# Kernel tuning notes

Measured on AMD Instinct MI355X. Metric: run time of the kernel, lower is better.

Reference implementation:

```python
import jax, jax.numpy as jnp
import numpy as np

NHEAD = 8

def layernorm(x, g, b, eps=1e-5):
    mu = x.mean(-1, keepdims=True)
    var = ((x - mu) ** 2).mean(-1, keepdims=True)
    return (x - mu) / jnp.sqrt(var + eps) * g + b

def linear_attention(q, k, v, eps=1e-6):
    # LoFTR kernelized linear attention: phi(x) = elu(x) + 1
    Q = jax.nn.elu(q) + 1.0          # [n, l, h, d]
    K = jax.nn.elu(k) + 1.0          # [n, s, h, d]
    s_len = v.shape[1]
    KV = jnp.einsum("nshd,nshv->nhdv", K, v / s_len)
    Z = 1.0 / (jnp.einsum("nlhd,nhd->nlh", Q, K.sum(axis=1)) + eps)
    return jnp.einsum("nlhd,nhdv,nlh->nlhv", Q, KV, Z) * s_len

def _block(x_base, q, k, v, Wm, W1, W2, g1, b1, g2, b2):
    bs, L, h, dh = q.shape
    msg = linear_attention(q, k, v).reshape(bs, L, h * dh)
    msg = layernorm(msg @ Wm, g1, b1)
    hcat = jnp.concatenate([x_base, msg], axis=2)          # [bs, L, 2*d]
    out = jax.nn.relu(hcat @ W1) @ W2
    return layernorm(out, g2, b2)

def setup_inputs() -> dict:
    key = jax.random.key(0)
    ks = jax.random.split(key, 8)
    bs, L, S, d = 8, 4800, 4800, 256
    w = lambda k, i, o: jax.random.normal(k, (i, o), jnp.float32) * 0.02
    return {
        "x": jax.random.normal(ks[0], (bs, L, d), jnp.float32),
        "source": jax.random.normal(ks[1], (bs, S, d), jnp.float32),
        "Wq": w(ks[2], d, d), "Wk": w(ks[3], d, d), "Wv": w(ks[4], d, d),
        "Wm": w(ks[5], d, d),
        "W1": w(ks[6], 2 * d, 2 * d), "W2": w(ks[7], 2 * d, d),
        "g1": jnp.ones((d,), jnp.float32), "b1": jnp.zeros((d,), jnp.float32),
        "g2": jnp.ones((d,), jnp.float32), "b2": jnp.zeros((d,), jnp.float32),
    }

def reference(x, source, Wq, Wk, Wv, Wm, W1, W2, g1, b1, g2, b2):
    bs, L, d = x.shape
    h = NHEAD
    dh = d // h
    q = (x @ Wq).reshape(bs, L, h, dh)
    k = (source @ Wk).reshape(bs, -1, h, dh)
    v = (source @ Wv).reshape(bs, -1, h, dh)
    # permute-then-view reinterpretations, exactly as in the torch code
    p13 = lambda t: t.transpose(0, 1, 3, 2).reshape(bs, -1, h, dh)  # permute(0,1,3,2)
    p21 = lambda t: t.transpose(0, 2, 1, 3).reshape(bs, -1, h, dh)  # permute(0,2,1,3)
    p32 = lambda t: t.transpose(0, 3, 2, 1).reshape(bs, -1, h, dh)  # permute(0,3,2,1)
    blk = lambda xb, qq, kk, vv: _block(xb, qq, kk, vv, Wm, W1, W2, g1, b1, g2, b2)
    m = blk(x, q, k, v)
    m3 = blk(x, p13(q), p13(k), p13(v))
    x_mid = x + 0.5 * (m + m3)
    m1 = blk(x_mid, p21(q), p21(k), p21(v))
    m2 = blk(x_mid, p32(q), p32(k), p32(v))
    return x_mid + 0.5 * (m1 + m2)
```

## Files before the change

kernel.cpp:

```cpp
#include <hip/hip_runtime.h>
#include <type_traits>
#include <cstdint>
#include <cstddef>

#define L_SEQ 4800
#define DMODEL 256
#define BS 8
#define MROWS (BS*L_SEQ)
#define PERBATCH (L_SEQ*DMODEL)
#define KVSET 67584

typedef __attribute__((ext_vector_type(8))) short bfrag8;
typedef __attribute__((ext_vector_type(4))) float floatx4;

__device__ __forceinline__ float bf2f(unsigned short u){
  union { unsigned int i; float f; } x; x.i = ((unsigned int)u) << 16; return x.f;
}
__device__ __forceinline__ unsigned short f2bf(float f){
  union { float f; unsigned int i; } x; x.f = f;
  x.i += 0x7fff + ((x.i >> 16) & 1);
  return (unsigned short)(x.i >> 16);
}
__device__ __forceinline__ float phi(float x){
  return x > 0.f ? x + 1.f : __expf(x);
}
__device__ __forceinline__ void gll16(const void* g, void* l){
  __builtin_amdgcn_global_load_lds((const __attribute__((address_space(1))) unsigned int*)g,
      (__attribute__((address_space(3))) unsigned int*)l, 16, 0, 0);
}

template<typename TC, bool RELU>
__global__ __launch_bounds__(256) void gemm_mfma(const unsigned short* __restrict__ A,
                                                 const unsigned short* __restrict__ Bt,
                                                 TC* __restrict__ C, int M, int N, int K){
  __shared__ unsigned short Al[128*32];
  __shared__ unsigned short Bl[128*32];
  const int tid  = threadIdx.x;
  const int lane = tid & 63;
  const int wave = tid >> 6;
  const int row0 = blockIdx.y << 7;
  const int col0 = blockIdx.x << 7;
  const int wr0  = (wave & 1) << 6;
  const int wc0  = (wave >> 1) << 6;

  floatx4 acc[4][4] = {};

  const int i0 = tid, i1 = tid + 256;
  const int r0 = i0 >> 2, s0 = i0 & 3;
  const int r1 = i1 >> 2, s1 = i1 & 3;
  const int m = lane & 15, q = lane >> 4;

  for (int k0 = 0; k0 < K; k0 += 32){
    const unsigned short* ga0 = A  + (size_t)(row0 + r0)*K + k0 + s0*8;
    const unsigned short* ga1 = A  + (size_t)(row0 + r1)*K + k0 + s1*8;
    const unsigned short* gb0 = Bt + (size_t)(col0 + r0)*K + k0 + s0*8;
    const unsigned short* gb1 = Bt + (size_t)(col0 + r1)*K + k0 + s1*8;
    gll16(ga0, Al + (size_t)i0*8);
    gll16(ga1, Al + (size_t)i1*8);
    gll16(gb0, Bl + (size_t)i0*8);
    gll16(gb1, Bl + (size_t)i1*8);
    __builtin_amdgcn_s_waitcnt(0);
    __syncthreads();

    bfrag8 af[4], bf[4];
    #pragma unroll
    for (int t = 0; t < 4; t++){
      af[t] = *(const bfrag8*)(Al + (size_t)(wr0 + t*16 + m)*32 + q*8);
      bf[t] = *(const bfrag8*)(Bl + (size_t)(wc0 + t*16 + m)*32 + q*8);
    }
    #pragma unroll
    for (int mt = 0; mt < 4; mt++)
      #pragma unroll
      for (int nt = 0; nt < 4; nt++)
        acc[mt][nt] = __builtin_amdgcn_mfma_f32_16x16x32_bf16(af[mt], bf[nt], acc[mt][nt], 0, 0, 0);
    __syncthreads();
  }

  #pragma unroll
  for (int mt = 0; mt < 4; mt++){
    #pragma unroll
    for (int nt = 0; nt < 4; nt++){
      const int col  = col0 + wc0 + nt*16 + m;
      const int rowb = row0 + wr0 + mt*16 + q*4;
      #pragma unroll
      for (int i = 0; i < 4; i++){
        float v = acc[mt][nt][i];
        if (RELU) v = v > 0.f ? v : 0.f;
        if constexpr (std::is_same<TC,float>::value) C[(size_t)(rowb+i)*N + col] = v;
        else                                         C[(size_t)(rowb+i)*N + col] = f2bf(v);
      }
    }
  }
}

__global__ __launch_bounds__(256) void wconv(const float* __restrict__ W, unsigned short* __restrict__ Wt,
                                             int kshift, int N){
  int idx = blockIdx.x*256 + threadIdx.x;
  int kk = idx & ((1 << kshift) - 1);
  int nn = idx >> kshift;
  Wt[idx] = f2bf(W[(size_t)kk*N + nn]);
}
__global__ __launch_bounds__(256) void conv_bf16(const float* __restrict__ in, unsigned short* __restrict__ out){
  int i = blockIdx.x*256 + threadIdx.x;
  float4 v = ((const float4*)in)[i];
  ushort4 o; o.x = f2bf(v.x); o.y = f2bf(v.y); o.z = f2bf(v.z); o.w = f2bf(v.w);
  ((ushort4*)out)[i] = o;
}

__global__ __launch_bounds__(256) void permute1(const unsigned short* __restrict__ sA, unsigned short* __restrict__ dA,
                                                const unsigned short* __restrict__ sB, unsigned short* __restrict__ dB){
  const unsigned short* s = blockIdx.z ? sB : sA;
  unsigned short*       d = blockIdx.z ? dB : dA;
  __shared__ unsigned short tile[1024];
  const int t = threadIdx.x;
  const size_t base = (size_t)blockIdx.x * 1024;
  #pragma unroll
  for (int i = 0; i < 4; i++) tile[i*256 + t] = s[base + i*256 + t];
  __syncthreads();
  const int pg = ((t & 7) << 5) + (t >> 3);
  #pragma unroll
  for (int i = 0; i < 4; i++) d[base + i*256 + t] = tile[i*256 + pg];
}

__global__ __launch_bounds__(256) void permute2(const unsigned short* __restrict__ sA, unsigned short* __restrict__ dA,
                                                const unsigned short* __restrict__ sB, unsigned short* __restrict__ dB){
  const unsigned short* s = blockIdx.z ? sB : sA;
  unsigned short*       d = blockIdx.z ? dB : dA;
  __shared__ unsigned short tile[64*256];
  const int t = threadIdx.x;
  const int rr0 = blockIdx.x * 64;
  const size_t boff = (size_t)blockIdx.y * PERBATCH;
  #pragma unroll
  for (int i = 0; i < 16; i++){
    int u = i*256 + t;
    *(ushort4*)&tile[u*4] = *(const ushort4*)&s[boff + (size_t)rr0*256 + (size_t)u*4];
  }
  __syncthreads();
  #pragma unroll
  for (int i = 0; i < 8; i++){
    #pragma unroll
    for (int w = 0; w < 2; w++){
      int u = w*256 + t;
      int rr = u >> 3, c4 = (u & 7) << 2;
      ushort4 v = *(const ushort4*)&tile[rr*256 + i*32 + c4];
      *(ushort4*)&d[boff + (size_t)i*153600 + (size_t)rr0*32 + (size_t)u*4] = v;
    }
  }
}

__global__ __launch_bounds__(256) void permute3(const unsigned short* __restrict__ sA, unsigned short* __restrict__ dA,
                                                const unsigned short* __restrict__ sB, unsigned short* __restrict__ dB){
  const unsigned short* s = blockIdx.z ? sB : sA;
  unsigned short*       d = blockIdx.z ? dB : dA;
  __shared__ unsigned short tile[64*258];
  const int t = threadIdx.x;
  const int ll0 = blockIdx.x * 64;
  const size_t boff = (size_t)blockIdx.y * PERBATCH;
  #pragma unroll
  for (int i = 0; i < 32; i++){
    int u = i*256 + t;
    int row = u >> 7, col = (u & 127) << 1;
    *(ushort2*)&tile[row*258 + col] = *(const ushort2*)&s[boff + (size_t)(ll0+row)*256 + col];
  }
  __syncthreads();
  const int cw = t >> 6;
  const int ll = t & 63;
  #pragma unroll
  for (int cc = 0; cc < 256; cc += 4){
    int c = cc + cw;
    int sigma = ((c & 31) << 3) + (c >> 5);
    d[boff + (size_t)sigma*4800 + ll0 + ll] = tile[ll*258 + c];
  }
}

__global__ __launch_bounds__(256) void attn_stats(const unsigned short* __restrict__ kq,
                                                  const unsigned short* __restrict__ vq,
                                                  float* __restrict__ KV, float* __restrict__ Ksum){
  const int chunk = blockIdx.x, h = blockIdx.y, n = blockIdx.z;
  const int t = threadIdx.x;
  const int d = t >> 3;
  const int w4 = (t & 7) << 2;
  const size_t boff = (size_t)n * PERBATCH;
  __shared__ float kb[8][32], vb[8][32];
  const int lr = t >> 5, lj = t & 31;
  float a0=0.f, a1=0.f, a2=0.f, a3=0.f, ks=0.f;
  const int s0 = chunk * 240;
  for (int s = s0; s < s0 + 240; s += 8){
    int srci = (s + lr)*256 + (h << 5) + lj;
    kb[lr][lj] = phi(bf2f(kq[boff + srci]));
    vb[lr][lj] = bf2f(vq[boff + srci]);
    __syncthreads();
    #pragma unroll
    for (int r = 0; r < 8; r++){
      float kd = kb[r][d];
      ks += kd;
      a0 += kd * vb[r][w4+0];
      a1 += kd * vb[r][w4+1];
      a2 += kd * vb[r][w4+2];
      a3 += kd * vb[r][w4+3];
    }
    __syncthreads();
  }
  float* kvp = KV + (size_t)((((n<<3)+h)<<5) + d)*32 + w4;
  atomicAdd(kvp+0, a0);
  atomicAdd(kvp+1, a1);
  atomicAdd(kvp+2, a2);
  atomicAdd(kvp+3, a3);
  if ((t & 7) == 0) atomicAdd(Ksum + (((n<<3)+h)<<5) + d, ks);
}

__global__ __launch_bounds__(256) void attn_fused(const unsigned short* __restrict__ qq,
                                                  const float* __restrict__ KV,
                                                  const float* __restrict__ Ksum,
                                                  const unsigned short* __restrict__ WmT,
                                                  const float* __restrict__ g1,
                                                  const float* __restrict__ b1,
                                                  unsigned short* __restrict__ hcat){
  __shared__ float kvs[8192];
  __shared__ char  msgL[32768];
  __shared__ char  pool[16384];
  const int t = threadIdx.x;
  const int n = blockIdx.y;
  const int row0 = blockIdx.x << 6;
  const size_t boff = (size_t)n * PERBATCH;

  #pragma unroll
  for (int i = 0; i < 32; i++) kvs[i*256 + t] = KV[(size_t)n*8192 + i*256 + t];
  const float kssv = Ksum[n*256 + t];

  const int h = t >> 5, w = t & 31;
  const float* kvh = kvs + h*1024;
  float* Qs = (float*)pool;

  for (int p = 0; p < 8; p++){
    #pragma unroll
    for (int r = 0; r < 8; r++)
      Qs[r*256 + t] = phi(bf2f(qq[boff + (size_t)(row0 + p*8 + r)*256 + t]));
    __syncthreads();

    float acc[8], den[8];
    #pragma unroll
    for (int r = 0; r < 8; r++){
      float dd = Qs[r*256 + t] * kssv;
      #pragma unroll
      for (int o = 1; o < 32; o <<= 1) dd += __shfl_xor(dd, o, 64);
      den[r] = dd + 1e-6f;
      acc[r] = 0.f;
    }
    #pragma unroll
    for (int d4 = 0; d4 < 8; d4++){
      const float k0v = kvh[(d4*4+0)*32 + w];
      const float k1v = kvh[(d4*4+1)*32 + w];
      const float k2v = kvh[(d4*4+2)*32 + w];
      const float k3v = kvh[(d4*4+3)*32 + w];
      #pragma unroll
      for (int r = 0; r < 8; r++){
        float4 qv = *(const float4*)&Qs[r*256 + h*32 + d4*4];
        acc[r] += qv.x*k0v + qv.y*k1v + qv.z*k2v + qv.w*k3v;
      }
    }
    #pragma unroll
    for (int r = 0; r < 8; r++){
      int lrow = p*8 + r;
      int byte = (lrow << 9) + (t << 1);
      byte ^= (lrow & 7) << 4;
      *(unsigned short*)(msgL + byte) = f2bf(acc[r] / den[r]);
    }
    __syncthreads();
  }

  const int wave = t >> 6, lane = t & 63, m = lane & 15, qd = lane >> 4;
  float gv[16], bv[16];
  #pragma unroll
  for (int nt = 0; nt < 16; nt++){ gv[nt] = g1[nt*16 + m]; bv[nt] = b1[nt*16 + m]; }

  floatx4 acc[16] = {};
  for (int ks = 0; ks < 8; ks++){
    const int k0 = ks << 5;
    #pragma unroll
    for (int i = 0; i < 4; i++){
      int u = (i << 8) + t;
      int c = u >> 2, q4 = u & 3;
      gll16(WmT + (size_t)c*256 + k0 + ((q4 ^ (c & 3)) << 3), pool + (u << 4));
    }
    asm volatile("s_waitcnt vmcnt(0)" ::: "memory");
    __builtin_amdgcn_s_barrier();
    asm volatile("" ::: "memory");
    const int arow = (wave << 4) + m;
    int abyte = (arow << 9) + (ks << 6) + (qd << 4);
    abyte ^= (m & 7) << 4;
    bfrag8 af = *(const bfrag8*)(msgL + abyte);
    #pragma unroll
    for (int nt = 0; nt < 16; nt++){
      int col = (nt << 4) + m;
      bfrag8 bf = *(const bfrag8*)(pool + col*64 + ((qd ^ (m & 3)) << 4));
      acc[nt] = __builtin_amdgcn_mfma_f32_16x16x32_bf16(af, bf, acc[nt], 0, 0, 0);
    }
    asm volatile("" ::: "memory");
    __builtin_amdgcn_s_barrier();
    asm volatile("" ::: "memory");
  }

  float mu[4], rs[4];
  #pragma unroll
  for (int i = 0; i < 4; i++){
    float s = 0.f, q = 0.f;
    #pragma unroll
    for (int nt = 0; nt < 16; nt++){ float v = acc[nt][i]; s += v; q += v*v; }
    #pragma unroll
    for (int o = 1; o < 16; o <<= 1){ s += __shfl_xor(s, o, 64); q += __shfl_xor(q, o, 64); }
    float mean = s * (1.f/256.f);
    float var  = q * (1.f/256.f) - mean*mean;
    mu[i] = mean; rs[i] = rsqrtf(var + 1e-5f);
  }
  #pragma unroll
  for (int nt = 0; nt < 16; nt++){
    #pragma unroll
    for (int i = 0; i < 4; i++){
      int row = (wave << 4) + (qd << 2) + i;
      int col = (nt << 4) + m;
      int byte = (row << 9) + (col << 1);
      byte ^= (row & 7) << 4;
      *(unsigned short*)(msgL + byte) = f2bf((acc[nt][i] - mu[i]) * rs[i] * gv[nt] + bv[nt]);
    }
  }
  __syncthreads();
  const size_t gbase = (size_t)(n*4800 + row0) * 512;
  #pragma unroll
  for (int i = 0; i < 16; i++){
    int u = (i << 8) + t;
    int row = u >> 6, j = u & 63;
    int byte = ((row << 9) + (j << 3)) ^ ((row & 7) << 4);
    *(ushort4*)(hcat + gbase + (size_t)row*512 + 256 + (j << 2)) = *(const ushort4*)(msgL + byte);
  }
}

__global__ __launch_bounds__(512) void ffn_fused(const unsigned short* __restrict__ hcat,
                                                 const unsigned short* __restrict__ W1T,
                                                 const unsigned short* __restrict__ W2T,
                                                 const float* __restrict__ g2,
                                                 const float* __restrict__ b2,
                                                 float* __restrict__ macc, int add){
  __shared__ char stg[73728];
  __shared__ char hidm[65536];
  const int tid = threadIdx.x;
  const int wave = tid >> 6, lane = tid & 63;
  const int rg = wave >> 1, ch = wave & 1;
  const int m = lane & 15, qd = lane >> 4;
  const int row0 = blockIdx.x << 6;

  float gv[8], bv[8];
  #pragma unroll
  for (int nt = 0; nt < 8; nt++){
    int col = (ch << 7) + nt*16 + m;
    gv[nt] = g2[col]; bv[nt] = b2[col];
  }

  auto stage1 = [&](int ks, int b){
    const int k0 = ks << 5;
    {
      int u = tid & 255;
      int r = u >> 2, q4 = u & 3;
      gll16(hcat + (size_t)(row0 + r)*512 + k0 + ((q4 ^ (r & 3)) << 3),
            stg + (b << 12) + (u << 4));
    }
    #pragma unroll
    for (int i = 0; i < 4; i++){
      int u = (i << 9) + tid;
      int c = u >> 2, q4 = u & 3;
      gll16(W1T + (size_t)c*512 + k0 + ((q4 ^ (c & 3)) << 3),
            stg + 8192 + (b << 15) + (u << 4));
    }
  };

  floatx4 acc1[16] = {};
  stage1(0, 0);
  asm volatile("s_waitcnt vmcnt(0)" ::: "memory");
  __builtin_amdgcn_s_barrier();
  asm volatile("" ::: "memory");
  for (int ks = 0; ks < 16; ks++){
    if (ks < 15) stage1(ks+1, (ks+1) & 1);
    const char* hb = stg + ((ks & 1) << 12);
    const char* wb = stg + 8192 + ((ks & 1) << 15);
    const int arow = (rg << 4) + m;
    bfrag8 af = *(const bfrag8*)(hb + arow*64 + ((qd ^ (m & 3)) << 4));
    #pragma unroll
    for (int nt = 0; nt < 16; nt++){
      int col = (ch << 8) + (nt << 4) + m;
      bfrag8 bf = *(const bfrag8*)(wb + col*64 + ((qd ^ (m & 3)) << 4));
      acc1[nt] = __builtin_amdgcn_mfma_f32_16x16x32_bf16(af, bf, acc1[nt], 0, 0, 0);
    }
    asm volatile("" ::: "memory");
    if (ks < 15) asm volatile("s_waitcnt vmcnt(0)" ::: "memory");
    __builtin_amdgcn_s_barrier();
    asm volatile("" ::: "memory");
  }

  #pragma unroll
  for (int nt = 0; nt < 16; nt++){
    #pragma unroll
    for (int i = 0; i < 4; i++){
      float v = acc1[nt][i];
      v = v > 0.f ? v : 0.f;
      int row = (rg << 4) + (qd << 2) + i;
      int col = (ch << 8) + (nt << 4) + m;
      int byte = (row << 10) + (col << 1);
      byte ^= (row & 7) << 4;
      *(unsigned short*)(hidm + byte) = f2bf(v);
    }
  }

  auto stage2 = [&](int ks, int b){
    const int k0 = ks << 5;
    #pragma unroll
    for (int i = 0; i < 2; i++){
      int u = (i << 9) + tid;
      int c = u >> 2, q4 = u & 3;
      gll16(W2T + (size_t)c*512 + k0 + ((q4 ^ (c & 3)) << 3),
            stg + (b << 14) + (u << 4));
    }
  };
  stage2(0, 0);
  asm volatile("s_waitcnt vmcnt(0) lgkmcnt(0)" ::: "memory");
  __builtin_amdgcn_s_barrier();
  asm volatile("" ::: "memory");

  floatx4 acc2[8] = {};
  for (int ks = 0; ks < 16; ks++){
    if (ks < 15) stage2(ks+1, (ks+1) & 1);
    const char* wb = stg + ((ks & 1) << 14);
    const int arow = (rg << 4) + m;
    int abyte = (arow << 10) + (ks << 6) + (qd << 4);
    abyte ^= (m & 7) << 4;
    bfrag8 af = *(const bfrag8*)(hidm + abyte);
    #pragma unroll
    for (int nt = 0; nt < 8; nt++){
      int col = (ch << 7) + (nt << 4) + m;
      bfrag8 bf = *(const bfrag8*)(wb + col*64 + ((qd ^ (m & 3)) << 4));
      acc2[nt] = __builtin_amdgcn_mfma_f32_16x16x32_bf16(af, bf, acc2[nt], 0, 0, 0);
    }
    asm volatile("" ::: "memory");
    if (ks < 15) asm volatile("s_waitcnt vmcnt(0)" ::: "memory");
    __builtin_amdgcn_s_barrier();
    asm volatile("" ::: "memory");
  }

  float2* LNp = (float2*)(stg + 32768);
  #pragma unroll
  for (int i = 0; i < 4; i++){
    float s = 0.f, q = 0.f;
    #pragma unroll
    for (int nt = 0; nt < 8; nt++){ float v = acc2[nt][i]; s += v; q += v*v; }
    #pragma unroll
    for (int o = 1; o < 16; o <<= 1){ s += __shfl_xor(s, o, 64); q += __shfl_xor(q, o, 64); }
    if (m == 0){
      int row = (rg << 4) + (qd << 2) + i;
      LNp[row*2 + ch] = make_float2(s, q);
    }
  }
  asm volatile("s_waitcnt lgkmcnt(0)" ::: "memory");
  __builtin_amdgcn_s_barrier();
  asm volatile("" ::: "memory");

  float mu[4], rs[4];
  #pragma unroll
  for (int i = 0; i < 4; i++){
    int row = (rg << 4) + (qd << 2) + i;
    float2 a = LNp[row*2], c = LNp[row*2 + 1];
    float S = a.x + c.x, Q = a.y + c.y;
    float mean = S * (1.f/256.f);
    float var  = Q * (1.f/256.f) - mean*mean;
    mu[i] = mean; rs[i] = rsqrtf(var + 1e-5f);
  }
  float* ysh = (float*)hidm;
  #pragma unroll
  for (int nt = 0; nt < 8; nt++){
    #pragma unroll
    for (int i = 0; i < 4; i++){
      int row = (rg << 4) + (qd << 2) + i;
      int col = (ch << 7) + (nt << 4) + m;
      ysh[(row << 8) + col] = (acc2[nt][i] - mu[i]) * rs[i] * gv[nt] + bv[nt];
    }
  }
  asm volatile("s_waitcnt lgkmcnt(0)" ::: "memory");
  __builtin_amdgcn_s_barrier();
  asm volatile("" ::: "memory");
  #pragma unroll
  for (int i = 0; i < 8; i++){
    int u = (i << 9) + tid;
    int row = u >> 6, c4 = u & 63;
    float4 v = *(const float4*)(ysh + (row << 8) + (c4 << 2));
    float4* gp = (float4*)(macc + (size_t)(row0 + row)*256) + c4;
    if (add){ float4 o = *gp; v.x += o.x; v.y += o.y; v.z += o.z; v.w += o.w; }
    *gp = v;
  }
}

__global__ __launch_bounds__(256) void fill_hcat(const float* __restrict__ x, unsigned short* __restrict__ hcat){
  size_t i = (size_t)blockIdx.x*256 + threadIdx.x;
  hcat[(i >> 8)*512 + (i & 255)] = f2bf(x[i]);
}
__global__ __launch_bounds__(256) void xmid_k(const float* __restrict__ x, const float* __restrict__ macc,
                                              float* __restrict__ xmid, unsigned short* __restrict__ hcat){
  size_t i = (size_t)blockIdx.x*256 + threadIdx.x;
  float v = x[i] + 0.5f*macc[i];
  xmid[i] = v;
  hcat[(i >> 8)*512 + (i & 255)] = f2bf(v);
}
__global__ __launch_bounds__(256) void final_k(float* __restrict__ out, const float* __restrict__ macc){
  size_t i = (size_t)blockIdx.x*256 + threadIdx.x;
  out[i] = out[i] + 0.5f*macc[i];
}
__global__ __launch_bounds__(256) void zero_k(float* __restrict__ p, int n){
  int i = blockIdx.x*256 + threadIdx.x;
  if (i < n) p[i] = 0.f;
}

extern "C" void kernel_launch(void* const* d_in, const int* in_sizes, int n_in,
                              void* d_out, int out_size, void* d_ws, size_t ws_size,
                              hipStream_t stream){
  const float* x   = (const float*)d_in[0];
  const float* src = (const float*)d_in[1];
  const float* Wq  = (const float*)d_in[2];
  const float* Wk  = (const float*)d_in[3];
  const float* Wv  = (const float*)d_in[4];
  const float* Wm  = (const float*)d_in[5];
  const float* W1  = (const float*)d_in[6];
  const float* W2  = (const float*)d_in[7];
  const float* g1  = (const float*)d_in[8];
  const float* b1  = (const float*)d_in[9];
  const float* g2  = (const float*)d_in[10];
  const float* b2  = (const float*)d_in[11];
  float* out = (float*)d_out;

  char* ws = (char*)d_ws;
  size_t off = 0;
  auto alloc = [&](size_t bytes) -> void* {
    void* p = ws + off;
    off += (bytes + 255) & ~(size_t)255;
    return p;
  };
  unsigned short* qB    = (unsigned short*)alloc((size_t)MROWS*256*2);
  unsigned short* kB    = (unsigned short*)alloc((size_t)MROWS*256*2);
  unsigned short* vB    = (unsigned short*)alloc((size_t)MROWS*256*2);
  unsigned short* hcatB = (unsigned short*)alloc((size_t)MROWS*512*2);
  float* t1   = (float*)alloc((size_t)MROWS*256*4);
  float* macc = (float*)alloc((size_t)MROWS*256*4);
  float* KV4  = (float*)alloc((size_t)4*KVSET*4);
  unsigned short* WqT = (unsigned short*)alloc((size_t)256*256*2);
  unsigned short* WkT = (unsigned short*)alloc((size_t)256*256*2);
  unsigned short* WvT = (unsigned short*)alloc((size_t)256*256*2);
  unsigned short* WmT = (unsigned short*)alloc((size_t)256*256*2);
  unsigned short* W1T = (unsigned short*)alloc((size_t)512*512*2);
  unsigned short* W2T = (unsigned short*)alloc((size_t)256*512*2);
  (void)ws_size; (void)in_sizes; (void)n_in; (void)out_size;

  unsigned short* srcbf = (unsigned short*)t1;
  unsigned short* xbf   = srcbf + (size_t)MROWS*256;
  unsigned short* qP    = (unsigned short*)t1;
  unsigned short* kP    = (unsigned short*)macc;
  unsigned short* vP    = kP + (size_t)MROWS*256;
  float* xmid = out;

  const dim3 blk(256);

  wconv<<<dim3(256),  blk, 0, stream>>>(Wq, WqT, 8, 256);
  wconv<<<dim3(256),  blk, 0, stream>>>(Wk, WkT, 8, 256);
  wconv<<<dim3(256),  blk, 0, stream>>>(Wv, WvT, 8, 256);
  wconv<<<dim3(256),  blk, 0, stream>>>(Wm, WmT, 8, 256);
  wconv<<<dim3(1024), blk, 0, stream>>>(W1, W1T, 9, 512);
  wconv<<<dim3(512),  blk, 0, stream>>>(W2, W2T, 9, 256);
  conv_bf16<<<dim3(9600), blk, 0, stream>>>(src, srcbf);
  conv_bf16<<<dim3(9600), blk, 0, stream>>>(x,   xbf);

  gemm_mfma<unsigned short, false><<<dim3(2,300), blk, 0, stream>>>(xbf,   WqT, qB, MROWS, 256, 256);
  gemm_mfma<unsigned short, false><<<dim3(2,300), blk, 0, stream>>>(srcbf, WkT, kB, MROWS, 256, 256);
  gemm_mfma<unsigned short, false><<<dim3(2,300), blk, 0, stream>>>(srcbf, WvT, vB, MROWS, 256, 256);

  zero_k<<<dim3(1056), blk, 0, stream>>>(KV4, 4*KVSET);
  attn_stats<<<dim3(20,8,8), blk, 0, stream>>>(kB, vB, KV4 + 0*KVSET, KV4 + 0*KVSET + 65536);
  permute1<<<dim3(9600,1,2), blk, 0, stream>>>(kB, kP, vB, vP);
  attn_stats<<<dim3(20,8,8), blk, 0, stream>>>(kP, vP, KV4 + 1*KVSET, KV4 + 1*KVSET + 65536);
  permute2<<<dim3(75,8,2),  blk, 0, stream>>>(kB, kP, vB, vP);
  attn_stats<<<dim3(20,8,8), blk, 0, stream>>>(kP, vP, KV4 + 2*KVSET, KV4 + 2*KVSET + 65536);
  permute3<<<dim3(75,8,2),  blk, 0, stream>>>(kB, kP, vB, vP);
  attn_stats<<<dim3(20,8,8), blk, 0, stream>>>(kP, vP, KV4 + 3*KVSET, KV4 + 3*KVSET + 65536);

  fill_hcat<<<dim3(MROWS), blk, 0, stream>>>(x, hcatB);

  auto run_block = [&](int mode, int add){
    const float* KV   = KV4 + (size_t)mode*KVSET;
    const float* Ksum = KV + 65536;
    const unsigned short* qsrc = qB;
    if (mode == 1){ permute1<<<dim3(9600,1,1), blk, 0, stream>>>(qB, qP, nullptr, nullptr); qsrc = qP; }
    else if (mode == 2){ permute2<<<dim3(75,8,1), blk, 0, stream>>>(qB, qP, nullptr, nullptr); qsrc = qP; }
    else if (mode == 3){ permute3<<<dim3(75,8,1), blk, 0, stream>>>(qB, qP, nullptr, nullptr); qsrc = qP; }
    attn_fused<<<dim3(75,BS), blk, 0, stream>>>(qsrc, KV, Ksum, WmT, g1, b1, hcatB);
    ffn_fused<<<dim3(600), dim3(512), 0, stream>>>(hcatB, W1T, W2T, g2, b2, macc, add);
  };

  run_block(0, 0);
  run_block(1, 1);
  xmid_k<<<dim3(MROWS), blk, 0, stream>>>(x, macc, xmid, hcatB);
  run_block(2, 0);
  run_block(3, 1);
  final_k<<<dim3(MROWS), blk, 0, stream>>>(out, macc);
}
```

Baseline: 1.108 ms.

## Double-buffer GEMM, shrink attention tiles, restructure fused FFN to cut LDS use

The generic GEMM now double-buffers its LDS tiles with XOR swizzling and uses one barrier per k-step. The attention kernel drops from 64 to 16 rows per block with 4x more blocks. It computes the denominator inline from a shared Ksum and reads Wm fragments straight from global memory. The FFN kernel drops its 64KB hidden buffer and streams hidden-activation chunks through the staging buffer while W2 loads, with each wave owning a column slice and launch bounds asking for more occupancy. Together these aim to raise occupancy and overlap, at the cost of more complex producer scheduling and redundant global Wm reads per block.

```diff
diff --git a/kernel.cpp b/kernel.cpp
--- a/kernel.cpp
+++ b/kernel.cpp
@@ -33,8 +33,8 @@
 __global__ __launch_bounds__(256) void gemm_mfma(const unsigned short* __restrict__ A,
                                                  const unsigned short* __restrict__ Bt,
                                                  TC* __restrict__ C, int M, int N, int K){
-  __shared__ unsigned short Al[128*32];
-  __shared__ unsigned short Bl[128*32];
+  __shared__ unsigned short Al[2][4096];
+  __shared__ unsigned short Bl[2][4096];
   const int tid  = threadIdx.x;
   const int lane = tid & 63;
   const int wave = tid >> 6;
@@ -42,38 +42,42 @@
   const int col0 = blockIdx.x << 7;
   const int wr0  = (wave & 1) << 6;
   const int wc0  = (wave >> 1) << 6;
+  const int m = lane & 15, q = lane >> 4;
+  const int sw = (m >> 1) & 3;
 
   floatx4 acc[4][4] = {};
 
-  const int i0 = tid, i1 = tid + 256;
-  const int r0 = i0 >> 2, s0 = i0 & 3;
-  const int r1 = i1 >> 2, s1 = i1 & 3;
-  const int m = lane & 15, q = lane >> 4;
-
-  for (int k0 = 0; k0 < K; k0 += 32){
-    const unsigned short* ga0 = A  + (size_t)(row0 + r0)*K + k0 + s0*8;
-    const unsigned short* ga1 = A  + (size_t)(row0 + r1)*K + k0 + s1*8;
-    const unsigned short* gb0 = Bt + (size_t)(col0 + r0)*K + k0 + s0*8;
-    const unsigned short* gb1 = Bt + (size_t)(col0 + r1)*K + k0 + s1*8;
-    gll16(ga0, Al + (size_t)i0*8);
-    gll16(ga1, Al + (size_t)i1*8);
-    gll16(gb0, Bl + (size_t)i0*8);
-    gll16(gb1, Bl + (size_t)i1*8);
-    __builtin_amdgcn_s_waitcnt(0);
-    __syncthreads();
-
+  const int u0 = tid, u1 = tid + 256;
+  const int r0 = u0 >> 2, s0 = u0 & 3;
+  const int r1 = u1 >> 2, s1 = u1 & 3;
+
+  auto stage = [&](int k0, int b){
+    gll16(A  + (size_t)(row0 + r0)*K + k0 + ((s0 ^ ((r0 >> 1) & 3)) << 3), Al[b] + (size_t)u0*8);
+    gll16(A  + (size_t)(row0 + r1)*K + k0 + ((s1 ^ ((r1 >> 1) & 3)) << 3), Al[b] + (size_t)u1*8);
+    gll16(Bt + (size_t)(col0 + r0)*K + k0 + ((s0 ^ ((r0 >> 1) & 3)) << 3), Bl[b] + (size_t)u0*8);
+    gll16(Bt + (size_t)(col0 + r1)*K + k0 + ((s1 ^ ((r1 >> 1) & 3)) << 3), Bl[b] + (size_t)u1*8);
+  };
+
+  stage(0, 0);
+  const int nk = K >> 5;
+  for (int ks = 0; ks < nk; ks++){
+    asm volatile("s_waitcnt vmcnt(0) lgkmcnt(0)" ::: "memory");
+    __builtin_amdgcn_s_barrier();
+    asm volatile("" ::: "memory");
+    if (ks < nk - 1) stage((ks + 1) << 5, (ks + 1) & 1);
+    const unsigned short* ab = Al[ks & 1];
+    const unsigned short* bb = Bl[ks & 1];
     bfrag8 af[4], bf[4];
     #pragma unroll
     for (int t = 0; t < 4; t++){
-      af[t] = *(const bfrag8*)(Al + (size_t)(wr0 + t*16 + m)*32 + q*8);
-      bf[t] = *(const bfrag8*)(Bl + (size_t)(wc0 + t*16 + m)*32 + q*8);
+      af[t] = *(const bfrag8*)(ab + (size_t)(wr0 + t*16 + m)*32 + ((q ^ sw) << 3));
+      bf[t] = *(const bfrag8*)(bb + (size_t)(wc0 + t*16 + m)*32 + ((q ^ sw) << 3));
     }
     #pragma unroll
     for (int mt = 0; mt < 4; mt++)
       #pragma unroll
       for (int nt = 0; nt < 4; nt++)
         acc[mt][nt] = __builtin_amdgcn_mfma_f32_16x16x32_bf16(af[mt], bf[nt], acc[mt][nt], 0, 0, 0);
-    __syncthreads();
   }
 
   #pragma unroll
@@ -217,283 +221,276 @@
                                                   const float* __restrict__ b1,
                                                   unsigned short* __restrict__ hcat){
   __shared__ float kvs[8192];
-  __shared__ char  msgL[32768];
-  __shared__ char  pool[16384];
+  __shared__ float Qs[4096];
+  __shared__ float kss[256];
+  __shared__ char  msgL[8192];
+  __shared__ float2 LNp[16][4];
   const int t = threadIdx.x;
   const int n = blockIdx.y;
-  const int row0 = blockIdx.x << 6;
+  const int row0 = blockIdx.x << 4;
   const size_t boff = (size_t)n * PERBATCH;
 
-  #pragma unroll
-  for (int i = 0; i < 32; i++) kvs[i*256 + t] = KV[(size_t)n*8192 + i*256 + t];
-  const float kssv = Ksum[n*256 + t];
-
-  const int h = t >> 5, w = t & 31;
-  const float* kvh = kvs + h*1024;
-  float* Qs = (float*)pool;
-
-  for (int p = 0; p < 8; p++){
-    #pragma unroll
-    for (int r = 0; r < 8; r++)
-      Qs[r*256 + t] = phi(bf2f(qq[boff + (size_t)(row0 + p*8 + r)*256 + t]));
-    __syncthreads();
-
-    float acc[8], den[8];
-    #pragma unroll
-    for (int r = 0; r < 8; r++){
-      float dd = Qs[r*256 + t] * kssv;
-      #pragma unroll
-      for (int o = 1; o < 32; o <<= 1) dd += __shfl_xor(dd, o, 64);
-      den[r] = dd + 1e-6f;
-      acc[r] = 0.f;
-    }
-    #pragma unroll
-    for (int d4 = 0; d4 < 8; d4++){
-      const float k0v = kvh[(d4*4+0)*32 + w];
-      const float k1v = kvh[(d4*4+1)*32 + w];
-      const float k2v = kvh[(d4*4+2)*32 + w];
-      const float k3v = kvh[(d4*4+3)*32 + w];
-      #pragma unroll
-      for (int r = 0; r < 8; r++){
-        float4 qv = *(const float4*)&Qs[r*256 + h*32 + d4*4];
-        acc[r] += qv.x*k0v + qv.y*k1v + qv.z*k2v + qv.w*k3v;
-      }
-    }
-    #pragma unroll
-    for (int r = 0; r < 8; r++){
-      int lrow = p*8 + r;
-      int byte = (lrow << 9) + (t << 1);
-      byte ^= (lrow & 7) << 4;
-      *(unsigned short*)(msgL + byte) = f2bf(acc[r] / den[r]);
-    }
-    __syncthreads();
-  }
-
-  const int wave = t >> 6, lane = t & 63, m = lane & 15, qd = lane >> 4;
-  float gv[16], bv[16];
-  #pragma unroll
-  for (int nt = 0; nt < 16; nt++){ gv[nt] = g1[nt*16 + m]; bv[nt] = b1[nt*16 + m]; }
-
-  floatx4 acc[16] = {};
-  for (int ks = 0; ks < 8; ks++){
-    const int k0 = ks << 5;
+  {
+    const float4* kvsrc = (const float4*)(KV + (size_t)n*8192);
+    #pragma unroll
+    for (int i = 0; i < 8; i++) ((float4*)kvs)[i*256 + t] = kvsrc[i*256 + t];
+    kss[t] = Ksum[n*256 + t];
     #pragma unroll
     for (int i = 0; i < 4; i++){
       int u = (i << 8) + t;
-      int c = u >> 2, q4 = u & 3;
-      gll16(WmT + (size_t)c*256 + k0 + ((q4 ^ (c & 3)) << 3), pool + (u << 4));
-    }
-    asm volatile("s_waitcnt vmcnt(0)" ::: "memory");
-    __builtin_amdgcn_s_barrier();
-    asm volatile("" ::: "memory");
-    const int arow = (wave << 4) + m;
-    int abyte = (arow << 9) + (ks << 6) + (qd << 4);
-    abyte ^= (m & 7) << 4;
+      int r = u >> 6, c4 = (u & 63) << 2;
+      ushort4 v = *(const ushort4*)(qq + boff + (size_t)(row0 + r)*256 + c4);
+      float4 f;
+      f.x = phi(bf2f(v.x)); f.y = phi(bf2f(v.y)); f.z = phi(bf2f(v.z)); f.w = phi(bf2f(v.w));
+      *(float4*)&Qs[r*256 + c4] = f;
+    }
+  }
+  __syncthreads();
+
+  {
+    const int h = t >> 5, w = t & 31;
+    const float* kvh = kvs + h*1024;
+    const float* ksh = kss + h*32;
+    float acc[16], den[16];
+    #pragma unroll
+    for (int r = 0; r < 16; r++){ acc[r] = 0.f; den[r] = 1e-6f; }
+    #pragma unroll
+    for (int d4 = 0; d4 < 8; d4++){
+      const float k0 = kvh[(d4*4+0)*32 + w];
+      const float k1 = kvh[(d4*4+1)*32 + w];
+      const float k2 = kvh[(d4*4+2)*32 + w];
+      const float k3 = kvh[(d4*4+3)*32 + w];
+      const float s0 = ksh[d4*4+0], s1 = ksh[d4*4+1], s2 = ksh[d4*4+2], s3 = ksh[d4*4+3];
+      #pragma unroll
+      for (int r = 0; r < 16; r++){
+        float4 qv = *(const float4*)&Qs[r*256 + h*32 + d4*4];
+        acc[r] += qv.x*k0 + qv.y*k1 + qv.z*k2 + qv.w*k3;
+        den[r] += qv.x*s0 + qv.y*s1 + qv.z*s2 + qv.w*s3;
+      }
+    }
+    #pragma unroll
+    for (int r = 0; r < 16; r++){
+      int byte = (r << 9) + ((t << 1) ^ ((r & 7) << 4));
+      *(unsigned short*)(msgL + byte) = f2bf(acc[r] / den[r]);
+    }
+  }
+  __syncthreads();
+
+  const int wv = t >> 6, lane = t & 63, m = lane & 15, qd = lane >> 4;
+  floatx4 Cf[4] = {};
+  #pragma unroll
+  for (int ks = 0; ks < 8; ks++){
+    int abyte = m*512 + ((ks*64 + qd*16) ^ ((m & 7) << 4));
     bfrag8 af = *(const bfrag8*)(msgL + abyte);
     #pragma unroll
-    for (int nt = 0; nt < 16; nt++){
-      int col = (nt << 4) + m;
-      bfrag8 bf = *(const bfrag8*)(pool + col*64 + ((qd ^ (m & 3)) << 4));
-      acc[nt] = __builtin_amdgcn_mfma_f32_16x16x32_bf16(af, bf, acc[nt], 0, 0, 0);
-    }
-    asm volatile("" ::: "memory");
-    __builtin_amdgcn_s_barrier();
-    asm volatile("" ::: "memory");
-  }
-
-  float mu[4], rs[4];
+    for (int nt = 0; nt < 4; nt++){
+      int col = wv*64 + nt*16 + m;
+      bfrag8 bf = *(const bfrag8*)(WmT + (size_t)col*256 + ks*32 + qd*8);
+      Cf[nt] = __builtin_amdgcn_mfma_f32_16x16x32_bf16(af, bf, Cf[nt], 0, 0, 0);
+    }
+  }
+
   #pragma unroll
   for (int i = 0; i < 4; i++){
     float s = 0.f, q = 0.f;
     #pragma unroll
-    for (int nt = 0; nt < 16; nt++){ float v = acc[nt][i]; s += v; q += v*v; }
+    for (int nt = 0; nt < 4; nt++){ float v = Cf[nt][i]; s += v; q += v*v; }
     #pragma unroll
     for (int o = 1; o < 16; o <<= 1){ s += __shfl_xor(s, o, 64); q += __shfl_xor(q, o, 64); }
-    float mean = s * (1.f/256.f);
-    float var  = q * (1.f/256.f) - mean*mean;
-    mu[i] = mean; rs[i] = rsqrtf(var + 1e-5f);
-  }
-  #pragma unroll
-  for (int nt = 0; nt < 16; nt++){
-    #pragma unroll
-    for (int i = 0; i < 4; i++){
-      int row = (wave << 4) + (qd << 2) + i;
-      int col = (nt << 4) + m;
-      int byte = (row << 9) + (col << 1);
-      byte ^= (row & 7) << 4;
-      *(unsigned short*)(msgL + byte) = f2bf((acc[nt][i] - mu[i]) * rs[i] * gv[nt] + bv[nt]);
-    }
-  }
-  __syncthreads();
-  const size_t gbase = (size_t)(n*4800 + row0) * 512;
-  #pragma unroll
-  for (int i = 0; i < 16; i++){
+    if (m == 0) LNp[qd*4 + i][wv] = make_float2(s, q);
+  }
+  __syncthreads();
+  float gv[4], bv[4];
+  #pragma unroll
+  for (int nt = 0; nt < 4; nt++){ int col = wv*64 + nt*16 + m; gv[nt] = g1[col]; bv[nt] = b1[col]; }
+  #pragma unroll
+  for (int i = 0; i < 4; i++){
+    int row = qd*4 + i;
+    float2 p0 = LNp[row][0], p1 = LNp[row][1], p2 = LNp[row][2], p3 = LNp[row][3];
+    float S = p0.x + p1.x + p2.x + p3.x;
+    float Q = p0.y + p1.y + p2.y + p3.y;
+    float mu = S * (1.f/256.f);
+    float rs = rsqrtf(Q * (1.f/256.f) - mu*mu + 1e-5f);
+    #pragma unroll
+    for (int nt = 0; nt < 4; nt++){
+      int col = wv*64 + nt*16 + m;
+      *(unsigned short*)(msgL + row*512 + col*2) = f2bf((Cf[nt][i] - mu) * rs * gv[nt] + bv[nt]);
+    }
+  }
+  __syncthreads();
+  const size_t gbase = ((size_t)n*4800 + row0)*512 + 256;
+  #pragma unroll
+  for (int i = 0; i < 4; i++){
     int u = (i << 8) + t;
-    int row = u >> 6, j = u & 63;
-    int byte = ((row << 9) + (j << 3)) ^ ((row & 7) << 4);
-    *(ushort4*)(hcat + gbase + (size_t)row*512 + 256 + (j << 2)) = *(const ushort4*)(msgL + byte);
-  }
-}
-
-__global__ __launch_bounds__(512) void ffn_fused(const unsigned short* __restrict__ hcat,
-                                                 const unsigned short* __restrict__ W1T,
-                                                 const unsigned short* __restrict__ W2T,
-                                                 const float* __restrict__ g2,
-                                                 const float* __restrict__ b2,
-                                                 float* __restrict__ macc, int add){
+    int r = u >> 6, c4 = (u & 63) << 2;
+    *(ushort4*)(hcat + gbase + (size_t)r*512 + c4) = *(const ushort4*)(msgL + r*512 + c4*2);
+  }
+}
+
+__global__ __launch_bounds__(512, 4) void ffn_fused(const unsigned short* __restrict__ hcat,
+                                                    const unsigned short* __restrict__ W1T,
+                                                    const unsigned short* __restrict__ W2T,
+                                                    const float* __restrict__ g2,
+                                                    const float* __restrict__ b2,
+                                                    float* __restrict__ macc, int add){
   __shared__ char stg[73728];
-  __shared__ char hidm[65536];
   const int tid = threadIdx.x;
-  const int wave = tid >> 6, lane = tid & 63;
-  const int rg = wave >> 1, ch = wave & 1;
+  const int wv = tid >> 6, lane = tid & 63;
   const int m = lane & 15, qd = lane >> 4;
+  const int sw = (m >> 1) & 3;
   const int row0 = blockIdx.x << 6;
-
-  float gv[8], bv[8];
-  #pragma unroll
-  for (int nt = 0; nt < 8; nt++){
-    int col = (ch << 7) + nt*16 + m;
-    gv[nt] = g2[col]; bv[nt] = b2[col];
-  }
 
   auto stage1 = [&](int ks, int b){
     const int k0 = ks << 5;
     {
       int u = tid & 255;
       int r = u >> 2, q4 = u & 3;
-      gll16(hcat + (size_t)(row0 + r)*512 + k0 + ((q4 ^ (r & 3)) << 3),
+      gll16(hcat + (size_t)(row0 + r)*512 + k0 + ((q4 ^ ((r >> 1) & 3)) << 3),
             stg + (b << 12) + (u << 4));
     }
     #pragma unroll
     for (int i = 0; i < 4; i++){
       int u = (i << 9) + tid;
-      int c = u >> 2, q4 = u & 3;
-      gll16(W1T + (size_t)c*512 + k0 + ((q4 ^ (c & 3)) << 3),
+      int r = u >> 2, q4 = u & 3;
+      gll16(W1T + (size_t)r*512 + k0 + ((q4 ^ ((r >> 1) & 3)) << 3),
             stg + 8192 + (b << 15) + (u << 4));
     }
   };
 
-  floatx4 acc1[16] = {};
+  floatx4 acc1[4][4] = {};
   stage1(0, 0);
-  asm volatile("s_waitcnt vmcnt(0)" ::: "memory");
-  __builtin_amdgcn_s_barrier();
-  asm volatile("" ::: "memory");
   for (int ks = 0; ks < 16; ks++){
-    if (ks < 15) stage1(ks+1, (ks+1) & 1);
+    asm volatile("s_waitcnt vmcnt(0) lgkmcnt(0)" ::: "memory");
+    __builtin_amdgcn_s_barrier();
+    asm volatile("" ::: "memory");
+    if (ks < 15) stage1(ks + 1, (ks + 1) & 1);
     const char* hb = stg + ((ks & 1) << 12);
     const char* wb = stg + 8192 + ((ks & 1) << 15);
-    const int arow = (rg << 4) + m;
-    bfrag8 af = *(const bfrag8*)(hb + arow*64 + ((qd ^ (m & 3)) << 4));
-    #pragma unroll
-    for (int nt = 0; nt < 16; nt++){
-      int col = (ch << 8) + (nt << 4) + m;
-      bfrag8 bf = *(const bfrag8*)(wb + col*64 + ((qd ^ (m & 3)) << 4));
-      acc1[nt] = __builtin_amdgcn_mfma_f32_16x16x32_bf16(af, bf, acc1[nt], 0, 0, 0);
-    }
-    asm volatile("" ::: "memory");
-    if (ks < 15) asm volatile("s_waitcnt vmcnt(0)" ::: "memory");
+    bfrag8 af[4], bf[4];
+    #pragma unroll
+    for (int t = 0; t < 4; t++){
+      af[t] = *(const bfrag8*)(hb + (t*16 + m)*64 + ((qd ^ sw) << 4));
+      bf[t] = *(const bfrag8*)(wb + (wv*64 + t*16 + m)*64 + ((qd ^ sw) << 4));
+    }
+    #pragma unroll
+    for (int mt = 0; mt < 4; mt++)
+      #pragma unroll
+      for (int nt = 0; nt < 4; nt++)
+        acc1[mt][nt] = __builtin_amdgcn_mfma_f32_16x16x32_bf16(af[mt], bf[nt], acc1[mt][nt], 0, 0, 0);
+  }
+
+  unsigned int hp[4][4][2];
+  #pragma unroll
+  for (int mt = 0; mt < 4; mt++)
+    #pragma unroll
+    for (int nt = 0; nt < 4; nt++)
+      #pragma unroll
+      for (int i2 = 0; i2 < 2; i2++){
+        float a = acc1[mt][nt][2*i2];     a = a > 0.f ? a : 0.f;
+        float c = acc1[mt][nt][2*i2+1];   c = c > 0.f ? c : 0.f;
+        hp[mt][nt][i2] = (unsigned int)f2bf(a) | ((unsigned int)f2bf(c) << 16);
+      }
+
+#define PRODUCE_HALF(CB, NT0)                                                        \
+  { _Pragma("unroll")                                                                \
+    for (int mt = 0; mt < 4; mt++){                                                  \
+      _Pragma("unroll")                                                              \
+      for (int j = 0; j < 2; j++){                                                   \
+        _Pragma("unroll")                                                            \
+        for (int i = 0; i < 4; i++){                                                 \
+          int row = mt*16 + qd*4 + i;                                                \
+          int kl  = j*16 + m;                                                        \
+          int byte = row*64 + ((((kl >> 3)) ^ ((row >> 1) & 3)) << 4) + ((kl & 7) << 1); \
+          unsigned short v = (unsigned short)(hp[mt][(NT0) + j][i >> 1] >> ((i & 1) << 4)); \
+          *(unsigned short*)((CB) + byte) = v;                                       \
+        }                                                                            \
+      }                                                                              \
+    }                                                                                \
+  }
+
+  auto produce = [&](int c){
+    if (wv == (c >> 1)){
+      char* cb = stg + ((c & 1) << 12);
+      if ((c & 1) == 0) PRODUCE_HALF(cb, 0)
+      else              PRODUCE_HALF(cb, 2)
+    }
+  };
+  auto stage2 = [&](int ks, int b){
+    const int k0 = ks << 5;
+    #pragma unroll
+    for (int i = 0; i < 2; i++){
+      int u = (i << 9) + tid;
+      int r = u >> 2, q4 = u & 3;
+      gll16(W2T + (size_t)r*512 + k0 + ((q4 ^ ((r >> 1) & 3)) << 3),
+            stg + 8192 + (b << 14) + (u << 4));
+    }
+  };
+
+  produce(0);
+  stage2(0, 0);
+  floatx4 acc2[4][2] = {};
+  for (int ks = 0; ks < 16; ks++){
+    asm volatile("s_waitcnt vmcnt(0) lgkmcnt(0)" ::: "memory");
     __builtin_amdgcn_s_barrier();
     asm volatile("" ::: "memory");
-  }
-
-  #pragma unroll
-  for (int nt = 0; nt < 16; nt++){
+    if (ks < 15){ stage2(ks + 1, (ks + 1) & 1); produce(ks + 1); }
+    const char* cb = stg + ((ks & 1) << 12);
+    const char* wb = stg + 8192 + ((ks & 1) << 14);
+    bfrag8 af[4], bf[2];
+    #pragma unroll
+    for (int t = 0; t < 4; t++)
+      af[t] = *(const bfrag8*)(cb + (t*16 + m)*64 + ((qd ^ sw) << 4));
+    #pragma unroll
+    for (int nt = 0; nt < 2; nt++)
+      bf[nt] = *(const bfrag8*)(wb + (wv*32 + nt*16 + m)*64 + ((qd ^ sw) << 4));
+    #pragma unroll
+    for (int mt = 0; mt < 4; mt++)
+      #pragma unroll
+      for (int nt = 0; nt < 2; nt++)
+        acc2[mt][nt] = __builtin_amdgcn_mfma_f32_16x16x32_bf16(af[mt], bf[nt], acc2[mt][nt], 0, 0, 0);
+  }
+
+  float2* LNp  = (float2*)(stg + 40960);
+  float2* LNmu = (float2*)(stg + 45056);
+  #pragma unroll
+  for (int mt = 0; mt < 4; mt++)
     #pragma unroll
     for (int i = 0; i < 4; i++){
-      float v = acc1[nt][i];
-      v = v > 0.f ? v : 0.f;
-      int row = (rg << 4) + (qd << 2) + i;
-      int col = (ch << 8) + (nt << 4) + m;
-      int byte = (row << 10) + (col << 1);
-      byte ^= (row & 7) << 4;
-      *(unsigned short*)(hidm + byte) = f2bf(v);
-    }
-  }
-
-  auto stage2 = [&](int ks, int b){
-    const int k0 = ks << 5;
-    #pragma unroll
-    for (int i = 0; i < 2; i++){
-      int u = (i << 9) + tid;
-      int c = u >> 2, q4 = u & 3;
-      gll16(W2T + (size_t)c*512 + k0 + ((q4 ^ (c & 3)) << 3),
-            stg + (b << 14) + (u << 4));
-    }
-  };
-  stage2(0, 0);
-  asm volatile("s_waitcnt vmcnt(0) lgkmcnt(0)" ::: "memory");
-  __builtin_amdgcn_s_barrier();
-  asm volatile("" ::: "memory");
-
-  floatx4 acc2[8] = {};
-  for (int ks = 0; ks < 16; ks++){
-    if (ks < 15) stage2(ks+1, (ks+1) & 1);
-    const char* wb = stg + ((ks & 1) << 14);
-    const int arow = (rg << 4) + m;
-    int abyte = (arow << 10) + (ks << 6) + (qd << 4);
-    abyte ^= (m & 7) << 4;
-    bfrag8 af = *(const bfrag8*)(hidm + abyte);
-    #pragma unroll
-    for (int nt = 0; nt < 8; nt++){
-      int col = (ch << 7) + (nt << 4) + m;
-      bfrag8 bf = *(const bfrag8*)(wb + col*64 + ((qd ^ (m & 3)) << 4));
-      acc2[nt] = __builtin_amdgcn_mfma_f32_16x16x32_bf16(af, bf, acc2[nt], 0, 0, 0);
-    }
-    asm volatile("" ::: "memory");
-    if (ks < 15) asm volatile("s_waitcnt vmcnt(0)" ::: "memory");
-    __builtin_amdgcn_s_barrier();
-    asm volatile("" ::: "memory");
-  }
-
-  float2* LNp = (float2*)(stg + 32768);
-  #pragma unroll
-  for (int i = 0; i < 4; i++){
-    float s = 0.f, q = 0.f;
-    #pragma unroll
-    for (int nt = 0; nt < 8; nt++){ float v = acc2[nt][i]; s += v; q += v*v; }
-    #pragma unroll
-    for (int o = 1; o < 16; o <<= 1){ s += __shfl_xor(s, o, 64); q += __shfl_xor(q, o, 64); }
-    if (m == 0){
-      int row = (rg << 4) + (qd << 2) + i;
-      LNp[row*2 + ch] = make_float2(s, q);
-    }
-  }
-  asm volatile("s_waitcnt lgkmcnt(0)" ::: "memory");
-  __builtin_amdgcn_s_barrier();
-  asm volatile("" ::: "memory");
-
-  float mu[4], rs[4];
-  #pragma unroll
-  for (int i = 0; i < 4; i++){
-    int row = (rg << 4) + (qd << 2) + i;
-    float2 a = LNp[row*2], c = LNp[row*2 + 1];
-    float S = a.x + c.x, Q = a.y + c.y;
+      float s = 0.f, q = 0.f;
+      #pragma unroll
+      for (int nt = 0; nt < 2; nt++){ float v = acc2[mt][nt][i]; s += v; q += v*v; }
+      #pragma unroll
+      for (int o = 1; o < 16; o <<= 1){ s += __shfl_xor(s, o, 64); q += __shfl_xor(q, o, 64); }
+      if (m == 0) LNp[(mt*16 + qd*4 + i)*8 + wv] = make_float2(s, q);
+    }
+  __syncthreads();
+  if (tid < 64){
+    float S = 0.f, Q = 0.f;
+    #pragma unroll
+    for (int j = 0; j < 8; j++){ float2 p = LNp[tid*8 + j]; S += p.x; Q += p.y; }
     float mean = S * (1.f/256.f);
     float var  = Q * (1.f/256.f) - mean*mean;
-    mu[i] = mean; rs[i] = rsqrtf(var + 1e-5f);
-  }
-  float* ysh = (float*)hidm;
-  #pragma unroll
-  for (int nt = 0; nt < 8; nt++){
+    LNmu[tid] = make_float2(mean, rsqrtf(var + 1e-5f));
+  }
+  __syncthreads();
+  float gv[2], bv[2];
+  #pragma unroll
+  for (int nt = 0; nt < 2; nt++){ int col = wv*32 + nt*16 + m; gv[nt] = g2[col]; bv[nt] = b2[col]; }
+  #pragma unroll
+  for (int mt = 0; mt < 4; mt++)
     #pragma unroll
     for (int i = 0; i < 4; i++){
-      int row = (rg << 4) + (qd << 2) + i;
-      int col = (ch << 7) + (nt << 4) + m;
-      ysh[(row << 8) + col] = (acc2[nt][i] - mu[i]) * rs[i] * gv[nt] + bv[nt];
-    }
-  }
-  asm volatile("s_waitcnt lgkmcnt(0)" ::: "memory");
-  __builtin_amdgcn_s_barrier();
-  asm volatile("" ::: "memory");
-  #pragma unroll
-  for (int i = 0; i < 8; i++){
-    int u = (i << 9) + tid;
-    int row = u >> 6, c4 = u & 63;
-    float4 v = *(const float4*)(ysh + (row << 8) + (c4 << 2));
-    float4* gp = (float4*)(macc + (size_t)(row0 + row)*256) + c4;
-    if (add){ float4 o = *gp; v.x += o.x; v.y += o.y; v.z += o.z; v.w += o.w; }
-    *gp = v;
-  }
+      int row = mt*16 + qd*4 + i;
+      float2 ms = LNmu[row];
+      #pragma unroll
+      for (int nt = 0; nt < 2; nt++){
+        float y = (acc2[mt][nt][i] - ms.x) * ms.y * gv[nt] + bv[nt];
+        float* p = macc + (size_t)(row0 + row)*256 + wv*32 + nt*16 + m;
+        if (add) y += *p;
+        *p = y;
+      }
+    }
+#undef PRODUCE_HALF
 }
 
 __global__ __launch_bounds__(256) void fill_hcat(const float* __restrict__ x, unsigned short* __restrict__ hcat){
@@ -595,7 +592,7 @@
     if (mode == 1){ permute1<<<dim3(9600,1,1), blk, 0, stream>>>(qB, qP, nullptr, nullptr); qsrc = qP; }
     else if (mode == 2){ permute2<<<dim3(75,8,1), blk, 0, stream>>>(qB, qP, nullptr, nullptr); qsrc = qP; }
     else if (mode == 3){ permute3<<<dim3(75,8,1), blk, 0, stream>>>(qB, qP, nullptr, nullptr); qsrc = qP; }
-    attn_fused<<<dim3(75,BS), blk, 0, stream>>>(qsrc, KV, Ksum, WmT, g1, b1, hcatB);
+    attn_fused<<<dim3(300,BS), blk, 0, stream>>>(qsrc, KV, Ksum, WmT, g1, b1, hcatB);
     ffn_fused<<<dim3(600), dim3(512), 0, stream>>>(hcatB, W1T, W2T, g2, b2, macc, add);
   };
 
```

New measurement: 1.326 ms. +19.7%, slower.
